# Optimization experiments

Measured on AMD Instinct MI355X. Metric: run time of the kernel, lower is better.

## Reference

```python
import jax, jax.numpy as jnp
import numpy as np

WINDOW = 4
EPS = 1e-5


def setup_inputs() -> dict:
    key = jax.random.key(0)
    ks = jax.random.split(key, 12)
    B, T, D = 2, 4096, 1024
    H = D // 2
    s = 0.02
    return {
        "x": jax.random.normal(ks[0], (B, T, D), dtype=jnp.float32),
        # tension_net: Linear(2D -> D/2), SiLU, Linear(D/2 -> 1). Weights stored [in, out].
        "w1": jax.random.normal(ks[1], (2 * D, H), dtype=jnp.float32) * s,
        "b1": jnp.zeros((H,), dtype=jnp.float32),
        "w2": jax.random.normal(ks[2], (H, 1), dtype=jnp.float32) * s,
        "b2": jnp.zeros((1,), dtype=jnp.float32),
        # wv: Linear(D -> D)
        "wv_w": jax.random.normal(ks[3], (D, D), dtype=jnp.float32) * s,
        "wv_b": jnp.zeros((D,), dtype=jnp.float32),
        # merge: Linear(2D -> D)
        "merge_w": jax.random.normal(ks[4], (2 * D, D), dtype=jnp.float32) * s,
        "merge_b": jnp.zeros((D,), dtype=jnp.float32),
        # LayerNorm(D)
        "gamma": jnp.ones((D,), dtype=jnp.float32),
        "beta": jnp.zeros((D,), dtype=jnp.float32),
    }


def reference(x, w1, b1, w2, b2, wv_w, wv_b, merge_w, merge_b, gamma, beta):
    B, T, D = x.shape
    W = WINDOW
    # Causal sliding-window neighbor gather: nb[:, t, w] = x[:, t-w-1] if t-w-1 >= 0 else 0.
    idx = jnp.arange(T)[:, None] - jnp.arange(W)[None, :] - 1          # [T, W]
    valid = (idx >= 0)                                                  # [T, W]
    nb = jnp.take(x, jnp.clip(idx, 0, None), axis=1)                   # [B, T, W, D]
    nb = jnp.where(valid[None, :, :, None], nb, jnp.zeros((), x.dtype))
    # Pairwise tension gate: tiny MLP on [h_t, nb].
    h_t = jnp.broadcast_to(x[:, :, None, :], (B, T, W, D))
    pair = jnp.concatenate([h_t, nb], axis=-1)                          # [B, T, W, 2D]
    hid = jax.nn.silu(jnp.einsum('btwe,eh->btwh', pair, w1) + b1)       # [B, T, W, D/2]
    tau = jax.nn.sigmoid((jnp.einsum('btwh,ho->btwo', hid, w2) + b2)[..., 0])  # [B, T, W]
    # Value projection of neighbors (note: zero-padded neighbors still get wv bias, matching torch).
    v = jnp.einsum('btwd,de->btwe', nb, wv_w) + wv_b                    # [B, T, W, D]
    msg = jnp.einsum('btw,btwd->btd', tau, v)                           # [B, T, D]
    # Merge + LayerNorm.
    y = jnp.einsum('bte,ed->btd', jnp.concatenate([x, msg], axis=-1), merge_w) + merge_b
    mu = jnp.mean(y, axis=-1, keepdims=True)
    var = jnp.mean(jnp.square(y - mu), axis=-1, keepdims=True)
    y = (y - mu) * jax.lax.rsqrt(var + EPS) * gamma + beta
    return y
```

## Files before the change

### kernel.cpp

```cpp
#include <hip/hip_runtime.h>
#include <hip/hip_bf16.h>

#define TT 4096
#define TD 1024
#define TM 8192
#define CN 3072
#define EPS 1e-5f

typedef __bf16 bf16;
typedef __bf16 bf16x4 __attribute__((ext_vector_type(4)));
typedef __bf16 bf16x8 __attribute__((ext_vector_type(8)));
typedef float  f32x4  __attribute__((ext_vector_type(4)));

#define GLOBAL_AS __attribute__((address_space(1)))
#define LDS_AS    __attribute__((address_space(3)))

__global__ __launch_bounds__(256) void prep_kernel(const float* __restrict__ x,
                                                   const float* __restrict__ w1,
                                                   const float* __restrict__ wv_w,
                                                   const float* __restrict__ wv_b,
                                                   const float* __restrict__ merge_w,
                                                   bf16* __restrict__ Xbf,
                                                   bf16* __restrict__ BigBT,
                                                   bf16* __restrict__ Amb,
                                                   bf16* __restrict__ WvBf,
                                                   float* __restrict__ cvecP) {
    __shared__ float tile[32][33];
    int b = blockIdx.x;
    const int tid = threadIdx.x;

    if (b < 16) {
        const int j = (b & 3) * 256 + tid;
        const int e0 = (b >> 2) * 256;
        const float* col = merge_w + (size_t)(1024 + e0) * 1024 + j;
        float acc = 0.f;
#pragma unroll 32
        for (int e = 0; e < 256; ++e) acc += wv_b[e0 + e] * col[(size_t)e * 1024];
        cvecP[(b >> 2) * 1024 + j] = acc;
        return;
    }
    b -= 16;
    if (b < 8192) {
        int i = b * 256 + tid;
        float4 v = ((const float4*)x)[i];
        bf16x4 o; o[0] = (bf16)v.x; o[1] = (bf16)v.y; o[2] = (bf16)v.z; o[3] = (bf16)v.w;
        *(bf16x4*)(Xbf + (size_t)i * 4) = o;
        return;
    }
    b -= 8192;

    const float* src; bf16* dst; int srcN, tilesX, dstOff;
    if (b < 512)       {            src = w1;                        srcN = 512;  tilesX = 16; dst = BigBT; dstOff = 0;    }
    else if (b < 1024) { b -= 512;  src = w1 + (size_t)1024 * 512;   srcN = 512;  tilesX = 16; dst = BigBT; dstOff = 512;  }
    else if (b < 2048) { b -= 1024; src = merge_w;                   srcN = 1024; tilesX = 32; dst = BigBT; dstOff = 2048; }
    else if (b < 3072) { b -= 2048; src = merge_w + (size_t)1024 * 1024; srcN = 1024; tilesX = 32; dst = Amb; dstOff = 0; }
    else {
        b -= 3072;
        int i = b * 256 + tid;
        float4 v = ((const float4*)wv_w)[i];
        bf16x4 o; o[0] = (bf16)v.x; o[1] = (bf16)v.y; o[2] = (bf16)v.z; o[3] = (bf16)v.w;
        *(bf16x4*)(WvBf + (size_t)i * 4) = o;
        return;
    }
    int n0 = (b % tilesX) * 32, k0 = (b / tilesX) * 32;
    int tx = tid & 31, ty = tid >> 5;
#pragma unroll
    for (int r = 0; r < 32; r += 8)
        tile[ty + r][tx] = src[(size_t)(k0 + ty + r) * srcN + n0 + tx];
    __syncthreads();
#pragma unroll
    for (int r = 0; r < 32; r += 8)
        dst[(size_t)(dstOff + n0 + ty + r) * 1024 + k0 + tx] = (bf16)tile[tx][ty + r];
}

__global__ __launch_bounds__(256) void wprime_kernel(const bf16* __restrict__ Amb,
                                                     const bf16* __restrict__ WvBf,
                                                     bf16* __restrict__ Wout,
                                                     const float* __restrict__ cvecP,
                                                     float* __restrict__ cvec) {
    int b = blockIdx.x;
    if (b == 256) {
        int j = threadIdx.x * 4;
        float4 s0 = *(const float4*)(cvecP + j);
        float4 s1 = *(const float4*)(cvecP + 1024 + j);
        float4 s2 = *(const float4*)(cvecP + 2048 + j);
        float4 s3 = *(const float4*)(cvecP + 3072 + j);
        float4 o = {s0.x + s1.x + s2.x + s3.x, s0.y + s1.y + s2.y + s3.y,
                    s0.z + s1.z + s2.z + s3.z, s0.w + s1.w + s2.w + s3.w};
        *(float4*)(cvec + j) = o;
        return;
    }
    __shared__ bf16 As[64 * 64];
    __shared__ bf16 Bs[64 * 64];
    const int m0 = (b >> 4) * 64;
    const int n0 = (b & 15) * 64;
    const int tid = threadIdx.x;
    const int wave = tid >> 6, lane = tid & 63;
    const int wr = (wave >> 1) * 32, wc = (wave & 1) * 32;
    const int lrow = lane & 15, cbase = lane >> 4;
    const int sw = lrow & 7;

    f32x4 acc[2][2] = {};

    for (int k0 = 0; k0 < 1024; k0 += 64) {
        __syncthreads();
#pragma unroll
        for (int c = 0; c < 2; ++c) {
            int e = (c * 256 + tid) * 8;
            int row = e >> 6;
            int q = (e >> 3) & 7;
            int gcol = ((q ^ (row & 7)) << 3);
            const bf16* ga = Amb  + (size_t)(m0 + row) * 1024 + k0 + gcol;
            const bf16* gb = WvBf + (size_t)(n0 + row) * 1024 + k0 + gcol;
            __builtin_amdgcn_global_load_lds((const GLOBAL_AS void*)ga,
                                             (LDS_AS void*)(As + e), 16, 0, 0);
            __builtin_amdgcn_global_load_lds((const GLOBAL_AS void*)gb,
                                             (LDS_AS void*)(Bs + e), 16, 0, 0);
        }
        __syncthreads();

#pragma unroll
        for (int kk = 0; kk < 2; ++kk) {
            const int qo = ((cbase + kk * 4) ^ sw) << 3;
            bf16x8 af[2], bfr[2];
#pragma unroll
            for (int i = 0; i < 2; ++i) {
                af[i]  = *(const bf16x8*)(As + (wr + i * 16 + lrow) * 64 + qo);
                bfr[i] = *(const bf16x8*)(Bs + (wc + i * 16 + lrow) * 64 + qo);
            }
#pragma unroll
            for (int i = 0; i < 2; ++i)
#pragma unroll
                for (int j = 0; j < 2; ++j)
                    acc[i][j] = __builtin_amdgcn_mfma_f32_16x16x32_bf16(af[i], bfr[j], acc[i][j], 0, 0, 0);
        }
    }

    const int lr = (lane >> 4) * 4, lc = lane & 15;
#pragma unroll
    for (int i = 0; i < 2; ++i)
#pragma unroll
        for (int j = 0; j < 2; ++j)
#pragma unroll
            for (int r = 0; r < 4; ++r)
                Wout[(size_t)(m0 + wr + i * 16 + lr + r) * 1024 + (n0 + wc + j * 16 + lc)]
                    = (bf16)acc[i][j][r];
}

#define MFMA16(a, b, c) __builtin_amdgcn_mfma_f32_16x16x32_bf16((a), (b), (c), 0, 0, 0)

#define STAGE_AB(BUF, T) do {                                                     \
    _Pragma("unroll")                                                             \
    for (int ld_ = 0; ld_ < 4; ++ld_) {                                           \
        const bf16* ga_ = aBase + (size_t)(ld_ * 64) * 1024 + (T) * 64;           \
        __builtin_amdgcn_global_load_lds((const GLOBAL_AS void*)ga_,              \
            (LDS_AS void*)(SMEM + (BUF) * 28672 + ld_ * 4096 + tid * 8), 16, 0, 0); \
    }                                                                             \
    _Pragma("unroll")                                                             \
    for (int ld_ = 0; ld_ < 3; ++ld_) {                                           \
        const bf16* gb_ = bBase + (size_t)(ld_ * 64) * 1024 + (T) * 64;           \
        __builtin_amdgcn_global_load_lds((const GLOBAL_AS void*)gb_,              \
            (LDS_AS void*)(SMEM + (BUF) * 28672 + 16384 + ld_ * 4096 + tid * 8), 16, 0, 0); \
    } } while (0)

#define AF(BUF, I, KK) (*(const bf16x8*)(SMEM + (BUF) * 28672 +                   \
    (wm * 64 + (I) * 16 + lrow) * 64 + (((cbase + (KK) * 4) ^ sw) << 3)))
#define BF(BUF, J, KK) (*(const bf16x8*)(SMEM + (BUF) * 28672 + 16384 +           \
    (wn * 96 + (J) * 16 + lrow) * 64 + (((cbase + (KK) * 4) ^ sw) << 3)))

#define NOSTAGE do {} while (0)

#define KTILE(BUF, STAGE_STMT) do {                                               \
    STAGE_STMT;                                                                   \
    _Pragma("unroll")                                                             \
    for (int kk = 0; kk < 2; ++kk) {                                              \
        bf16x8 bfr[6];                                                            \
        _Pragma("unroll")                                                         \
        for (int j = 0; j < 6; ++j) bfr[j] = BF(BUF, j, kk);                      \
        _Pragma("unroll")                                                         \
        for (int i = 0; i < 4; ++i) {                                             \
            bf16x8 a_ = AF(BUF, i, kk);                                           \
            _Pragma("unroll")                                                     \
            for (int j = 0; j < 6; ++j)                                           \
                acc[i][j] = MFMA16(a_, bfr[j], acc[i][j]);                        \
        }                                                                         \
    }                                                                             \
    asm volatile("s_waitcnt vmcnt(0)" ::: "memory");                              \
    __builtin_amdgcn_sched_barrier(0);                                            \
    __builtin_amdgcn_s_barrier();                                                 \
    __builtin_amdgcn_sched_barrier(0);                                            \
} while (0)

__global__ __launch_bounds__(512, 1) void gemm_big(const bf16* __restrict__ A,
                                                   const bf16* __restrict__ BT,
                                                   bf16* __restrict__ C) {
    __shared__ __align__(16) bf16 SMEM[57344];
    const int NB = 3072, K = 1024;

    const int L = blockIdx.x;
    const int m0 = (L >> 4) * 256;
    const int n0 = ((L & 7) * 2 + ((L >> 3) & 1)) * 192;
    const int tid = threadIdx.x;
    const int wave = tid >> 6, lane = tid & 63;
    const int wm = wave >> 1;
    const int wn = wave & 1;
    const int lrow = lane & 15, cbase = lane >> 4;
    const int sw = lrow & 7;

    const int r0 = tid >> 3;
    const int c0 = ((tid & 7) ^ ((tid >> 3) & 7)) << 3;
    const bf16* aBase = A  + (size_t)(m0 + r0) * K + c0;
    const bf16* bBase = BT + (size_t)(n0 + r0) * K + c0;

    f32x4 acc[4][6] = {};

    STAGE_AB(0, 0);
    asm volatile("s_waitcnt vmcnt(0)" ::: "memory");
    __builtin_amdgcn_sched_barrier(0);
    __builtin_amdgcn_s_barrier();
    __builtin_amdgcn_sched_barrier(0);

    for (int i = 0; i < 7; ++i) {
        const int t1 = 2 * i + 1, t2 = 2 * i + 2;
        KTILE(0, STAGE_AB(1, t1));
        KTILE(1, STAGE_AB(0, t2));
    }
    KTILE(0, STAGE_AB(1, 15));
    KTILE(1, NOSTAGE);

    __syncthreads();
    bf16* ep = SMEM + wave * 6656;
    const int lr = (lane >> 4) * 4, lc = lane & 15;
#pragma unroll
    for (int i = 0; i < 4; ++i)
#pragma unroll
        for (int j = 0; j < 6; ++j)
#pragma unroll
            for (int r = 0; r < 4; ++r)
                ep[(i * 16 + lr + r) * 104 + (j * 16 + lc)] = (bf16)acc[i][j][r];
    __syncthreads();

    bf16* Cw = C + (size_t)(m0 + wm * 64) * NB + n0 + wn * 96;
#pragma unroll
    for (int p = 0; p < 8; ++p) {
        int R = p * 8 + (lane >> 3);
        int Ccol = (lane & 7) * 8;
        bf16x8 v = *(const bf16x8*)(ep + R * 104 + Ccol);
        *(bf16x8*)(Cw + (size_t)R * NB + Ccol) = v;
    }
#pragma unroll
    for (int p = 0; p < 4; ++p) {
        int R = p * 16 + (lane >> 2);
        int Ccol = 64 + (lane & 3) * 8;
        bf16x8 v = *(const bf16x8*)(ep + R * 104 + Ccol);
        *(bf16x8*)(Cw + (size_t)R * NB + Ccol) = v;
    }
}

__global__ __launch_bounds__(256) void final_kernel(const bf16* __restrict__ C,
                                                    const float* __restrict__ b1,
                                                    const float* __restrict__ b2,
                                                    const float* __restrict__ w2,
                                                    const float* __restrict__ cvec,
                                                    const float* __restrict__ merge_b,
                                                    const float* __restrict__ gamma,
                                                    const float* __restrict__ beta,
                                                    float* __restrict__ out) {
    const int wave = threadIdx.x >> 6, lane = threadIdx.x & 63;
    const int row = blockIdx.x * 4 + wave;
    const int t = row & (TT - 1);
    const bf16* Crow = C + (size_t)row * CN;

    const int h0 = lane * 8;
    bf16x8 u8 = *(const bf16x8*)(Crow + h0);
    float4 b1a = *(const float4*)(b1 + h0), b1b = *(const float4*)(b1 + h0 + 4);
    float4 w2a = *(const float4*)(w2 + h0), w2b = *(const float4*)(w2 + h0 + 4);
    float u[8] = {(float)u8[0] + b1a.x, (float)u8[1] + b1a.y,
                  (float)u8[2] + b1a.z, (float)u8[3] + b1a.w,
                  (float)u8[4] + b1b.x, (float)u8[5] + b1b.y,
                  (float)u8[6] + b1b.z, (float)u8[7] + b1b.w};
    const float w2v[8] = {w2a.x, w2a.y, w2a.z, w2a.w, w2b.x, w2b.y, w2b.z, w2b.w};

    float partial[4];
#pragma unroll
    for (int w = 0; w < 4; ++w) {
        float p = 0.f;
        if (t >= w + 1) {
            bf16x8 v8 = *(const bf16x8*)(C + (size_t)(row - w - 1) * CN + 512 + h0);
#pragma unroll
            for (int k = 0; k < 8; ++k) {
                float z = u[k] + (float)v8[k];
                p += (z / (1.f + __expf(-z))) * w2v[k];
            }
        } else {
#pragma unroll
            for (int k = 0; k < 8; ++k) {
                float z = u[k];
                p += (z / (1.f + __expf(-z))) * w2v[k];
            }
        }
        partial[w] = p;
    }
#pragma unroll
    for (int w = 0; w < 4; ++w)
#pragma unroll
        for (int off = 1; off < 64; off <<= 1)
            partial[w] += __shfl_xor(partial[w], off, 64);

    const float bias2 = b2[0];
    float taus[4];
#pragma unroll
    for (int w = 0; w < 4; ++w)
        taus[w] = 1.f / (1.f + __expf(-(partial[w] + bias2)));
    const float tsum = taus[0] + taus[1] + taus[2] + taus[3];

    const int d0 = lane * 16;
    bf16x8 y1a = *(const bf16x8*)(Crow + 2048 + d0);
    bf16x8 y1b = *(const bf16x8*)(Crow + 2048 + d0 + 8);
    float v[16];
#pragma unroll
    for (int k = 0; k < 8; ++k) { v[k] = (float)y1a[k]; v[8 + k] = (float)y1b[k]; }
#pragma unroll
    for (int q = 0; q < 4; ++q) {
        float4 cv = *(const float4*)(cvec + d0 + q * 4);
        float4 mb = *(const float4*)(merge_b + d0 + q * 4);
        v[q*4+0] += tsum * cv.x + mb.x; v[q*4+1] += tsum * cv.y + mb.y;
        v[q*4+2] += tsum * cv.z + mb.z; v[q*4+3] += tsum * cv.w + mb.w;
    }
#pragma unroll
    for (int w = 0; w < 4; ++w) {
        if (t >= w + 1) {
            const bf16* Pn = C + (size_t)(row - w - 1) * CN + 1024 + d0;
            bf16x8 pa = *(const bf16x8*)Pn;
            bf16x8 pb = *(const bf16x8*)(Pn + 8);
#pragma unroll
            for (int k = 0; k < 8; ++k) {
                v[k] += taus[w] * (float)pa[k];
                v[8 + k] += taus[w] * (float)pb[k];
            }
        }
    }

    float s = 0.f, ss = 0.f;
#pragma unroll
    for (int k = 0; k < 16; ++k) { s += v[k]; ss += v[k] * v[k]; }
#pragma unroll
    for (int off = 1; off < 64; off <<= 1) {
        s  += __shfl_xor(s, off, 64);
        ss += __shfl_xor(ss, off, 64);
    }
    const float mu = s * (1.f / TD);
    const float var = ss * (1.f / TD) - mu * mu;
    const float r = rsqrtf(var + EPS);

#pragma unroll
    for (int q = 0; q < 4; ++q) {
        float4 g  = *(const float4*)(gamma + d0 + q * 4);
        float4 bt = *(const float4*)(beta + d0 + q * 4);
        float4 o;
        o.x = (v[q*4+0] - mu) * r * g.x + bt.x;
        o.y = (v[q*4+1] - mu) * r * g.y + bt.y;
        o.z = (v[q*4+2] - mu) * r * g.z + bt.z;
        o.w = (v[q*4+3] - mu) * r * g.w + bt.w;
        *(float4*)(out + (size_t)row * TD + d0 + q * 4) = o;
    }
}

extern "C" void kernel_launch(void* const* d_in, const int* in_sizes, int n_in,
                              void* d_out, int out_size, void* d_ws, size_t ws_size,
                              hipStream_t stream) {
    const float* x       = (const float*)d_in[0];
    const float* w1      = (const float*)d_in[1];
    const float* b1      = (const float*)d_in[2];
    const float* w2      = (const float*)d_in[3];
    const float* b2      = (const float*)d_in[4];
    const float* wv_w    = (const float*)d_in[5];
    const float* wv_b    = (const float*)d_in[6];
    const float* merge_w = (const float*)d_in[7];
    const float* merge_b = (const float*)d_in[8];
    const float* gamma   = (const float*)d_in[9];
    const float* beta    = (const float*)d_in[10];
    float* out = (float*)d_out;

    char* ws = (char*)d_ws;
    bf16*  Xbf   = (bf16*)ws;  ws += (size_t)TM * 1024 * 2;
    bf16*  BigBT = (bf16*)ws;  ws += (size_t)CN * 1024 * 2;
    bf16*  Amb   = (bf16*)ws;  ws += (size_t)1024 * 1024 * 2;
    bf16*  WvBf  = (bf16*)ws;  ws += (size_t)1024 * 1024 * 2;
    float* cvecP = (float*)ws; ws += (size_t)4 * 1024 * 4;
    float* cvec  = (float*)ws; ws += (size_t)1024 * 4;
    bf16*  Cbuf  = (bf16*)ws;

    prep_kernel<<<12304, 256, 0, stream>>>(x, w1, wv_w, wv_b, merge_w,
                                           Xbf, BigBT, Amb, WvBf, cvecP);

    wprime_kernel<<<257, 256, 0, stream>>>(Amb, WvBf, BigBT + (size_t)1024 * 1024,
                                           cvecP, cvec);

    gemm_big<<<512, 512, 0, stream>>>(Xbf, BigBT, Cbuf);

    final_kernel<<<TM / 4, 256, 0, stream>>>(Cbuf, b1, b2, w2, cvec, merge_b,
                                             gamma, beta, out);
}
```

Measured before the change: 200.9 us.

## Load GEMM A fragments directly into registers and shrink block tile to 128x192

The main GEMM no longer stages A through LDS. Each wave now loads its A fragments straight from global memory into double-buffered registers, while only B is staged in LDS with global_load_lds. The block tile shrinks from 256x192 with 512 threads to 128x192 with 256 threads, and launch bounds allow two blocks per CU. The wait before the barrier is relaxed to vmcnt(8), so the A prefetch can still be in flight when the barrier is reached. This cuts LDS footprint and LDS read traffic for A, at the cost of duplicated global/L2 reads of A across the two column waves and higher register pressure.

```diff
diff --git a/kernel.cpp b/kernel.cpp
--- a/kernel.cpp
+++ b/kernel.cpp
@@ -149,29 +149,30 @@
 
 #define MFMA16(a, b, c) __builtin_amdgcn_mfma_f32_16x16x32_bf16((a), (b), (c), 0, 0, 0)
 
-#define STAGE_AB(BUF, T) do {                                                     \
+#define STAGE_B(BUF, T) do {                                                      \
     _Pragma("unroll")                                                             \
-    for (int ld_ = 0; ld_ < 4; ++ld_) {                                           \
-        const bf16* ga_ = aBase + (size_t)(ld_ * 64) * 1024 + (T) * 64;           \
-        __builtin_amdgcn_global_load_lds((const GLOBAL_AS void*)ga_,              \
-            (LDS_AS void*)(SMEM + (BUF) * 28672 + ld_ * 4096 + tid * 8), 16, 0, 0); \
-    }                                                                             \
+    for (int ld_ = 0; ld_ < 6; ++ld_) {                                           \
+        const bf16* gb_ = bBase + (size_t)(ld_ * 32) * 1024 + (T) * 64;           \
+        __builtin_amdgcn_global_load_lds((const GLOBAL_AS void*)gb_,              \
+            (LDS_AS void*)(SMEM + (BUF) * 12288 + ld_ * 2048 + tid * 8), 16, 0, 0); \
+    } } while (0)
+
+#define BF(BUF, J, KK) (*(const bf16x8*)(SMEM + (BUF) * 12288 +                   \
+    (wn * 96 + (J) * 16 + lrow) * 64 + (((cbase + (KK) * 4) ^ sw) << 3)))
+
+#define LOAD_A(DST, T) do {                                                       \
     _Pragma("unroll")                                                             \
-    for (int ld_ = 0; ld_ < 3; ++ld_) {                                           \
-        const bf16* gb_ = bBase + (size_t)(ld_ * 64) * 1024 + (T) * 64;           \
-        __builtin_amdgcn_global_load_lds((const GLOBAL_AS void*)gb_,              \
-            (LDS_AS void*)(SMEM + (BUF) * 28672 + 16384 + ld_ * 4096 + tid * 8), 16, 0, 0); \
-    } } while (0)
-
-#define AF(BUF, I, KK) (*(const bf16x8*)(SMEM + (BUF) * 28672 +                   \
-    (wm * 64 + (I) * 16 + lrow) * 64 + (((cbase + (KK) * 4) ^ sw) << 3)))
-#define BF(BUF, J, KK) (*(const bf16x8*)(SMEM + (BUF) * 28672 + 16384 +           \
-    (wn * 96 + (J) * 16 + lrow) * 64 + (((cbase + (KK) * 4) ^ sw) << 3)))
-
-#define NOSTAGE do {} while (0)
-
-#define KTILE(BUF, STAGE_STMT) do {                                               \
-    STAGE_STMT;                                                                   \
+    for (int i_ = 0; i_ < 4; ++i_)                                                \
+        _Pragma("unroll")                                                         \
+        for (int kk_ = 0; kk_ < 2; ++kk_)                                         \
+            DST[i_ * 2 + kk_] = *(const bf16x8*)(aPtr +                           \
+                (size_t)(i_ * 16) * 1024 + (T) * 64 + kk_ * 32);                  \
+} while (0)
+
+#define GATE8 do { asm volatile("s_waitcnt vmcnt(8)" ::: "memory");               \
+                   __builtin_amdgcn_sched_barrier(0); } while (0)
+
+#define KTBODY(BUF, ACUR)                                                         \
     _Pragma("unroll")                                                             \
     for (int kk = 0; kk < 2; ++kk) {                                              \
         bf16x8 bfr[6];                                                            \
@@ -179,26 +180,29 @@
         for (int j = 0; j < 6; ++j) bfr[j] = BF(BUF, j, kk);                      \
         _Pragma("unroll")                                                         \
         for (int i = 0; i < 4; ++i) {                                             \
-            bf16x8 a_ = AF(BUF, i, kk);                                           \
             _Pragma("unroll")                                                     \
             for (int j = 0; j < 6; ++j)                                           \
-                acc[i][j] = MFMA16(a_, bfr[j], acc[i][j]);                        \
+                acc[i][j] = MFMA16(ACUR[i * 2 + kk], bfr[j], acc[i][j]);          \
         }                                                                         \
-    }                                                                             \
-    asm volatile("s_waitcnt vmcnt(0)" ::: "memory");                              \
-    __builtin_amdgcn_sched_barrier(0);                                            \
+    }
+
+#define KT(BUF, ACUR, ANXT, TN) do {                                              \
+    STAGE_B(1 - (BUF), TN);                                                       \
+    LOAD_A(ANXT, TN);                                                             \
+    KTBODY(BUF, ACUR);                                                            \
+    GATE8;                                                                        \
     __builtin_amdgcn_s_barrier();                                                 \
     __builtin_amdgcn_sched_barrier(0);                                            \
 } while (0)
 
-__global__ __launch_bounds__(512, 1) void gemm_big(const bf16* __restrict__ A,
+__global__ __launch_bounds__(256, 2) void gemm_big(const bf16* __restrict__ A,
                                                    const bf16* __restrict__ BT,
                                                    bf16* __restrict__ C) {
-    __shared__ __align__(16) bf16 SMEM[57344];
+    __shared__ __align__(16) bf16 SMEM[26624];
     const int NB = 3072, K = 1024;
 
     const int L = blockIdx.x;
-    const int m0 = (L >> 4) * 256;
+    const int m0 = (L >> 4) * 128;
     const int n0 = ((L & 7) * 2 + ((L >> 3) & 1)) * 192;
     const int tid = threadIdx.x;
     const int wave = tid >> 6, lane = tid & 63;
@@ -207,26 +211,28 @@
     const int lrow = lane & 15, cbase = lane >> 4;
     const int sw = lrow & 7;
 
+    const bf16* aPtr = A + (size_t)(m0 + wm * 64 + lrow) * K + cbase * 8;
+
     const int r0 = tid >> 3;
-    const int c0 = ((tid & 7) ^ ((tid >> 3) & 7)) << 3;
-    const bf16* aBase = A  + (size_t)(m0 + r0) * K + c0;
+    const int c0 = ((tid & 7) ^ (r0 & 7)) << 3;
     const bf16* bBase = BT + (size_t)(n0 + r0) * K + c0;
 
     f32x4 acc[4][6] = {};
-
-    STAGE_AB(0, 0);
-    asm volatile("s_waitcnt vmcnt(0)" ::: "memory");
-    __builtin_amdgcn_sched_barrier(0);
+    bf16x8 aA[8], aB[8];
+
+    STAGE_B(0, 0);
+    LOAD_A(aA, 0);
+    GATE8;
     __builtin_amdgcn_s_barrier();
     __builtin_amdgcn_sched_barrier(0);
 
     for (int i = 0; i < 7; ++i) {
         const int t1 = 2 * i + 1, t2 = 2 * i + 2;
-        KTILE(0, STAGE_AB(1, t1));
-        KTILE(1, STAGE_AB(0, t2));
-    }
-    KTILE(0, STAGE_AB(1, 15));
-    KTILE(1, NOSTAGE);
+        KT(0, aA, aB, t1);
+        KT(1, aB, aA, t2);
+    }
+    KT(0, aA, aB, 15);
+    KTBODY(1, aB);
 
     __syncthreads();
     bf16* ep = SMEM + wave * 6656;
@@ -397,7 +403,7 @@
     wprime_kernel<<<257, 256, 0, stream>>>(Amb, WvBf, BigBT + (size_t)1024 * 1024,
                                            cvecP, cvec);
 
-    gemm_big<<<512, 512, 0, stream>>>(Xbf, BigBT, Cbuf);
+    gemm_big<<<1024, 256, 0, stream>>>(Xbf, BigBT, Cbuf);
 
     final_kernel<<<TM / 4, 256, 0, stream>>>(Cbuf, b1, b2, w2, cvec, merge_b,
                                              gamma, beta, out);
```

New measurement: 224.3 us. 11.6% more time.
